# Performance work log

Hardware: AMD Instinct MI355X
Metric: run time of the kernel (lower is better)

Reference implementation:

```python
import jax, jax.numpy as jnp
import numpy as np

N_NODES = 100000
N_EDGES = 2000000
IN_C = 64
OUT_C = 64
K = 27
G = 4


def setup_inputs() -> dict:
    key = jax.random.key(0)
    k1, k2, k3, k4, k5, k6 = jax.random.split(key, 6)
    inp = {
        "input": jax.random.normal(k1, (N_NODES, IN_C), dtype=jnp.float32),
        "i": jax.random.randint(k2, (N_EDGES,), 0, N_NODES),
        "j": jax.random.randint(k3, (N_EDGES,), 0, N_NODES),
        "k": jax.random.randint(k4, (N_EDGES,), 0, K),
        "n": N_NODES,
        "weight": jax.random.normal(k5, (IN_C, OUT_C // G, K), dtype=jnp.float32) * 0.1,
        "bias": jax.random.normal(k6, (OUT_C,), dtype=jnp.float32) * 0.1,
    }
    return inp


def reference(input, i, j, k, n, weight, bias):
    # weight: [in_c, out_c//g, K] -> w: [K, g, in_c//g, out_c//g]
    w = weight.reshape(G, IN_C // G, OUT_C // G, K).transpose(3, 0, 1, 2)
    x3 = input.reshape(input.shape[0], G, IN_C // G)  # [n, g, c]
    # Transform every node by every kernel-position weight once (n*K small GEMMs)
    # instead of materializing a per-edge [E,g,c,d] weight gather.
    x_all = jnp.einsum('ngc,kgcd->nkgd', x3, w)  # [n, K, g, d]
    msgs = x_all[j, k]                            # [E, g, d] gather per edge
    out = jax.ops.segment_sum(msgs, i, num_segments=n)  # scatter-add to dst nodes
    out = out.reshape(-1, OUT_C) + bias
    return out
```

## Files before the change

### kernel.cpp

```cpp
#include <hip/hip_runtime.h>
#include <hip/hip_bf16.h>


#define KPOS 27
#define WPACK_UINTS (KPOS * 512)
#define SCAN_NB 256

typedef unsigned u32x4 __attribute__((ext_vector_type(4)));

__device__ __forceinline__ unsigned packbf(float a, float b) {
    unsigned ua = (unsigned)__bfloat16_as_ushort(__float2bfloat16(a));
    unsigned ub = (unsigned)__bfloat16_as_ushort(__float2bfloat16(b));
    return ua | (ub << 16);
}

#define DOT2(A, X, W) asm("v_dot2_f32_bf16 %0, %1, %2, %0" : "+v"(A) : "v"(X), "v"(W))

__global__ void init_out_kernel(float* __restrict__ out, const float* __restrict__ bias, int total) {
    int idx = blockIdx.x * blockDim.x + threadIdx.x;
    if (idx < total) out[idx] = bias[idx & 63];
}
__global__ void edge_kernel_rawW(const float* __restrict__ input, const int* __restrict__ ei,
                                 const int* __restrict__ ej, const int* __restrict__ ek,
                                 const float* __restrict__ weight, float* __restrict__ out, int n_edges) {
    const int lane = threadIdx.x & 63;
    const int g16 = lane & 48;
    const int d = lane & 15;
    int wave = (blockIdx.x * blockDim.x + threadIdx.x) >> 6;
    int n_waves = (gridDim.x * blockDim.x) >> 6;
    for (int e = wave; e < n_edges; e += n_waves) {
        int ie = ei[e], je = ej[e], ke = ek[e];
        float x = input[je * 64 + lane];
        float acc = 0.0f;
        #pragma unroll
        for (int c = 0; c < 16; ++c)
            acc += __shfl(x, g16 + c, 64) * weight[(g16 + c) * 432 + d * 27 + ke];
        atomicAdd(out + ie * 64 + lane, acc);
    }
}

__global__ void prep_kernel(const float* __restrict__ input, const float* __restrict__ weight,
                            unsigned* __restrict__ xb, unsigned* __restrict__ wp,
                            int* __restrict__ cnt, int n_nodes, int nquads) {
    int t = blockIdx.x * blockDim.x + threadIdx.x;
    if (t < n_nodes) cnt[t] = 0;
    if (t < WPACK_UINTS) {
        int k  = t >> 9;
        int r  = t & 511;
        int q  = r >> 8;
        int r2 = r & 255;
        int gc = r2 >> 2;
        int m  = r2 & 3;
        int g = gc >> 4, d = gc & 15;
        int c = (q * 4 + m) * 2;
        int ic = g * 16 + c;
        float f0 = weight[ic * 432 + d * 27 + k];
        float f1 = weight[(ic + 1) * 432 + d * 27 + k];
        wp[t] = packbf(f0, f1);
    }
    if (t < nquads) {
        const float4* in4 = (const float4*)input;
        float4 a = in4[2 * t], b = in4[2 * t + 1];
        uint4 o;
        o.x = packbf(a.x, a.y);
        o.y = packbf(a.z, a.w);
        o.z = packbf(b.x, b.y);
        o.w = packbf(b.z, b.w);
        ((uint4*)xb)[t] = o;
    }
}

__global__ void rank_kernel(const int* __restrict__ ei, int* __restrict__ cnt,
                            unsigned short* __restrict__ rank, int n_edges) {
    int e = blockIdx.x * blockDim.x + threadIdx.x;
    if (e < n_edges)
        rank[e] = (unsigned short)atomicAdd(&cnt[ei[e]], 1);
}

__global__ void scanA_kernel(const int* __restrict__ cnt, int* __restrict__ partial,
                             int n, int chunk) {
    __shared__ int red[256];
    int b = blockIdx.x;
    int lo = b * chunk, hi = min(lo + chunk, n);
    int s = 0;
    for (int v = lo + threadIdx.x; v < hi; v += 256) s += cnt[v];
    red[threadIdx.x] = s;
    __syncthreads();
    for (int d = 128; d > 0; d >>= 1) {
        if (threadIdx.x < d) red[threadIdx.x] += red[threadIdx.x + d];
        __syncthreads();
    }
    if (threadIdx.x == 0) partial[b] = red[0];
}

__global__ void scanB_kernel(int* __restrict__ partial, int* __restrict__ off, int n) {
    __shared__ int sums[SCAN_NB];
    int t = threadIdx.x;
    sums[t] = partial[t];
    __syncthreads();
    for (int d = 1; d < SCAN_NB; d <<= 1) {
        int val = (t >= d) ? sums[t - d] : 0;
        __syncthreads();
        sums[t] += val;
        __syncthreads();
    }
    partial[t] = (t == 0) ? 0 : sums[t - 1];
    if (t == SCAN_NB - 1) off[n] = sums[t];
}

__global__ void scanC_kernel(const int* __restrict__ cnt, const int* __restrict__ partial,
                             int* __restrict__ off, int n, int chunk) {
    __shared__ int excl[256];
    int b = blockIdx.x;
    int lo = b * chunk, hi = min(lo + chunk, n);
    int per = (chunk + 255) >> 8;
    int tlo = lo + threadIdx.x * per;
    int thi = min(tlo + per, hi);
    int s = 0;
    for (int v = tlo; v < thi; ++v) s += cnt[v];
    excl[threadIdx.x] = s;
    __syncthreads();
    for (int d = 1; d < 256; d <<= 1) {
        int val = (threadIdx.x >= d) ? excl[threadIdx.x - d] : 0;
        __syncthreads();
        excl[threadIdx.x] += val;
        __syncthreads();
    }
    int run = partial[b] + ((threadIdx.x == 0) ? 0 : excl[threadIdx.x - 1]);
    for (int v = tlo; v < thi; ++v) { off[v] = run; run += cnt[v]; }
}

__global__ void fill_kernel(const int* __restrict__ ei, const int* __restrict__ ej,
                            const int* __restrict__ ek, const int* __restrict__ off,
                            const unsigned short* __restrict__ rank,
                            unsigned* __restrict__ jk, int n_edges) {
    int e = blockIdx.x * blockDim.x + threadIdx.x;
    if (e < n_edges)
        jk[off[ei[e]] + (int)rank[e]] = (unsigned)ej[e] | ((unsigned)ek[e] << 17);
}

__launch_bounds__(1024, 8)
__global__ void gather_kernel(const unsigned* __restrict__ xb,
                              const unsigned* __restrict__ jk,
                              const int* __restrict__ off,
                              const unsigned* __restrict__ wp,
                              const float* __restrict__ bias,
                              float* __restrict__ out, int n) {
    __shared__ unsigned lds[WPACK_UINTS];
    for (int t = threadIdx.x; t < WPACK_UINTS / 4; t += blockDim.x)
        ((uint4*)lds)[t] = ((const uint4*)wp)[t];
    __syncthreads();

    const int lane = threadIdx.x & 63;
    const int g8   = (lane & 48) >> 1;
    const float b  = bias[lane];
    const unsigned* wl = lds + (lane << 2);

    int wid = (blockIdx.x * blockDim.x + threadIdx.x) >> 6;
    int nw  = (gridDim.x * blockDim.x) >> 6;

#define XISSUE(P0, P1, XA, XC, XB2, XD) do {                                     \
        const u32x4* xp0_ = (const u32x4*)(xb + (((P0) & 0x1FFFFu) << 5) + g8);  \
        const u32x4* xp1_ = (const u32x4*)(xb + (((P1) & 0x1FFFFu) << 5) + g8);  \
        XA  = xp0_[0]; XC = xp0_[1];                                             \
        XB2 = xp1_[0]; XD = xp1_[1];                                             \
    } while (0)

#define PAIR_EDGE(XA, XC, PV, AL, AH) do {                                       \
        const u32x4* wr_ = (const u32x4*)(wl + (((PV) >> 17) << 9));             \
        u32x4 wa_ = wr_[0], wb_ = wr_[64];                                       \
        DOT2(AL, XA[0], wa_[0]); DOT2(AH, XA[1], wa_[1]);                        \
        DOT2(AL, XA[2], wa_[2]); DOT2(AH, XA[3], wa_[3]);                        \
        DOT2(AL, XC[0], wb_[0]); DOT2(AH, XC[1], wb_[1]);                        \
        DOT2(AL, XC[2], wb_[2]); DOT2(AH, XC[3], wb_[3]);                        \
    } while (0)

    for (int v = wid; v < n; v += nw) {
        int e0 = off[v];
        int e1 = off[v + 1];
        int nE = e1 - e0;
        int P  = nE >> 1;
        float a0l = 0.0f, a0h = 0.0f, a1l = 0.0f, a1h = 0.0f;

        if (P > 0) {
            unsigned pc0 = jk[e0], pc1 = jk[e0 + 1];
            u32x4 Aa, Ac, Ab, Ad;
            XISSUE(pc0, pc1, Aa, Ac, Ab, Ad);
            unsigned pn0 = pc0, pn1 = pc1;
            if (P > 1) { pn0 = jk[e0 + 2]; pn1 = jk[e0 + 3]; }
            u32x4 Ba, Bc, Bb, Bd;

            int t = 0;
            for (; t + 2 <= P; t += 2) {
                unsigned pf0 = pn0, pf1 = pn1;
                if (t + 2 < P) { pf0 = jk[e0 + 2 * t + 4]; pf1 = jk[e0 + 2 * t + 5]; }
                XISSUE(pn0, pn1, Ba, Bc, Bb, Bd);
                PAIR_EDGE(Aa, Ac, pc0, a0l, a0h);
                PAIR_EDGE(Ab, Ad, pc1, a1l, a1h);
                pc0 = pn0; pc1 = pn1; pn0 = pf0; pn1 = pf1;
                unsigned pg0 = pn0, pg1 = pn1;
                if (t + 3 < P) { pg0 = jk[e0 + 2 * t + 6]; pg1 = jk[e0 + 2 * t + 7]; }
                if (t + 2 < P) XISSUE(pn0, pn1, Aa, Ac, Ab, Ad);
                PAIR_EDGE(Ba, Bc, pc0, a0l, a0h);
                PAIR_EDGE(Bb, Bd, pc1, a1l, a1h);
                pc0 = pn0; pc1 = pn1; pn0 = pg0; pn1 = pg1;
            }
            if (t < P) {
                PAIR_EDGE(Aa, Ac, pc0, a0l, a0h);
                PAIR_EDGE(Ab, Ad, pc1, a1l, a1h);
            }
        }

        if (nE & 1) {
            unsigned p_ = jk[e1 - 1];
            const u32x4* xr_ = (const u32x4*)(xb + ((p_ & 0x1FFFFu) << 5) + g8);
            u32x4 xa_ = xr_[0], xc_ = xr_[1];
            PAIR_EDGE(xa_, xc_, p_, a0l, a0h);
        }

        out[(v << 6) + lane] = (a0l + a0h) + (a1l + a1h) + b;
    }
#undef XISSUE
#undef PAIR_EDGE
}

static inline size_t al256(size_t x) { return (x + 255) & ~(size_t)255; }

extern "C" void kernel_launch(void* const* d_in, const int* in_sizes, int n_in,
                              void* d_out, int out_size, void* d_ws, size_t ws_size,
                              hipStream_t stream) {
    const float* input  = (const float*)d_in[0];
    const int*   ei     = (const int*)d_in[1];
    const int*   ej     = (const int*)d_in[2];
    const int*   ek     = (const int*)d_in[3];
    const float* weight = (const float*)d_in[5];
    const float* bias   = (const float*)d_in[6];

    const int n_edges = in_sizes[1];
    const int n_nodes = out_size / 64;

    size_t off_o  = 0;
    size_t off_s  = al256((size_t)(n_nodes + 1) * 4);
    size_t cnt_o  = off_o + off_s;
    size_t cnt_s  = al256((size_t)n_nodes * 4);
    size_t par_o  = cnt_o + cnt_s;
    size_t par_s  = al256((size_t)SCAN_NB * 4);
    size_t rank_o = par_o + par_s;
    size_t rank_s = al256((size_t)n_edges * 2);
    size_t jk_o   = rank_o + rank_s;
    size_t jk_s   = al256((size_t)n_edges * 4);
    size_t wp_o   = jk_o + jk_s;
    size_t wp_s   = al256((size_t)WPACK_UINTS * 4);
    size_t xb_o   = wp_o + wp_s;
    size_t xb_s   = al256((size_t)n_nodes * 64 * 2);
    size_t need   = xb_o + xb_s;

    if (ws_size < need) {
        int blocks = (out_size + 255) / 256;
        hipLaunchKernelGGL(init_out_kernel, dim3(blocks), dim3(256), 0, stream,
                           (float*)d_out, bias, out_size);
        hipLaunchKernelGGL(edge_kernel_rawW, dim3(2048), dim3(256), 0, stream,
                           input, ei, ej, ek, weight, (float*)d_out, n_edges);
        return;
    }

    char* ws = (char*)d_ws;
    int*            off  = (int*)(ws + off_o);
    int*            cnt  = (int*)(ws + cnt_o);
    int*            par  = (int*)(ws + par_o);
    unsigned short* rank = (unsigned short*)(ws + rank_o);
    unsigned*       jk   = (unsigned*)(ws + jk_o);
    unsigned*       wp   = (unsigned*)(ws + wp_o);
    unsigned*       xb   = (unsigned*)(ws + xb_o);

    const int eb = (n_edges + 255) / 256;
    const int nquads = n_nodes * 8;
    const int prep_range = max(nquads, max(n_nodes, WPACK_UINTS));
    const int chunk = (n_nodes + SCAN_NB - 1) / SCAN_NB;

    hipLaunchKernelGGL(prep_kernel, dim3((prep_range + 255) / 256), dim3(256), 0, stream,
                       input, weight, xb, wp, cnt, n_nodes, nquads);
    hipLaunchKernelGGL(rank_kernel, dim3(eb), dim3(256), 0, stream, ei, cnt, rank, n_edges);
    hipLaunchKernelGGL(scanA_kernel, dim3(SCAN_NB), dim3(256), 0, stream, cnt, par, n_nodes, chunk);
    hipLaunchKernelGGL(scanB_kernel, dim3(1), dim3(SCAN_NB), 0, stream, par, off, n_nodes);
    hipLaunchKernelGGL(scanC_kernel, dim3(SCAN_NB), dim3(256), 0, stream, cnt, par, off, n_nodes, chunk);
    hipLaunchKernelGGL(fill_kernel, dim3(eb), dim3(256), 0, stream, ei, ej, ek, off, rank, jk, n_edges);

    hipLaunchKernelGGL(gather_kernel, dim3(512), dim3(1024), 0, stream,
                       xb, jk, off, wp, bias, (float*)d_out, n_nodes);
}
```

Baseline: 304.5 us.

## Bucket edges by destination block and kernel position, accumulate in LDS

Edges are now counting-sorted into buckets keyed by (destination node block of 128, kernel position) instead of by destination node. Each 512-thread gather block owns 128 destination nodes and keeps a 128x64 fp32 accumulator in LDS. Its waves walk the block's edges grouped by kernel position, so each weight slice is loaded into registers once per run rather than reread from LDS per edge. Partial sums go to LDS through shared-memory atomics, then bias is added and the tile is written out with coalesced stores. The trade is LDS atomic contention in place of register accumulation, plus per-edge load imbalance across blocks.

New measurement: 978.7 us. 3.21x slower.

```diff
diff --git a/kernel.cpp b/kernel.cpp
--- a/kernel.cpp
+++ b/kernel.cpp
@@ -3,6 +3,7 @@
 
 
 #define KPOS 27
+#define NB 128
 #define WPACK_UINTS (KPOS * 512)
 #define SCAN_NB 256
 
@@ -41,9 +42,9 @@
 
 __global__ void prep_kernel(const float* __restrict__ input, const float* __restrict__ weight,
                             unsigned* __restrict__ xb, unsigned* __restrict__ wp,
-                            int* __restrict__ cnt, int n_nodes, int nquads) {
+                            int* __restrict__ cnt, int nbk, int nquads) {
     int t = blockIdx.x * blockDim.x + threadIdx.x;
-    if (t < n_nodes) cnt[t] = 0;
+    if (t < nbk) cnt[t] = 0;
     if (t < WPACK_UINTS) {
         int k  = t >> 9;
         int r  = t & 511;
@@ -70,11 +71,14 @@
     }
 }
 
-__global__ void rank_kernel(const int* __restrict__ ei, int* __restrict__ cnt,
+__global__ void rank_kernel(const int* __restrict__ ei, const int* __restrict__ ek,
+                            int* __restrict__ cnt,
                             unsigned short* __restrict__ rank, int n_edges) {
     int e = blockIdx.x * blockDim.x + threadIdx.x;
-    if (e < n_edges)
-        rank[e] = (unsigned short)atomicAdd(&cnt[ei[e]], 1);
+    if (e < n_edges) {
+        int bkt = (ei[e] >> 7) * KPOS + ek[e];
+        rank[e] = (unsigned short)atomicAdd(&cnt[bkt], 1);
+    }
 }
 
 __global__ void scanA_kernel(const int* __restrict__ cnt, int* __restrict__ partial,
@@ -133,95 +137,111 @@
 __global__ void fill_kernel(const int* __restrict__ ei, const int* __restrict__ ej,
                             const int* __restrict__ ek, const int* __restrict__ off,
                             const unsigned short* __restrict__ rank,
-                            unsigned* __restrict__ jk, int n_edges) {
+                            unsigned* __restrict__ recs, int n_edges) {
     int e = blockIdx.x * blockDim.x + threadIdx.x;
-    if (e < n_edges)
-        jk[off[ei[e]] + (int)rank[e]] = (unsigned)ej[e] | ((unsigned)ek[e] << 17);
-}
-
-__launch_bounds__(1024, 8)
+    if (e < n_edges) {
+        int ie = ei[e];
+        int bkt = (ie >> 7) * KPOS + ek[e];
+        recs[off[bkt] + (int)rank[e]] = (unsigned)ej[e] | (((unsigned)ie & (NB - 1)) << 17);
+    }
+}
+
+__launch_bounds__(512, 8)
 __global__ void gather_kernel(const unsigned* __restrict__ xb,
-                              const unsigned* __restrict__ jk,
-                              const int* __restrict__ off,
+                              const unsigned* __restrict__ recs,
+                              const int* __restrict__ boff,
                               const unsigned* __restrict__ wp,
                               const float* __restrict__ bias,
-                              float* __restrict__ out, int n) {
-    __shared__ unsigned lds[WPACK_UINTS];
-    for (int t = threadIdx.x; t < WPACK_UINTS / 4; t += blockDim.x)
-        ((uint4*)lds)[t] = ((const uint4*)wp)[t];
-    __syncthreads();
+                              float* __restrict__ out, int n_nodes) {
+    __shared__ float acc[NB * 64];
+    for (int t = threadIdx.x; t < NB * 16; t += blockDim.x)
+        ((float4*)acc)[t] = make_float4(0.f, 0.f, 0.f, 0.f);
+    __syncthreads();
+
+    const int b = blockIdx.x;
+    const int* bo = boff + b * KPOS;
+    const int seg1 = bo[KPOS];
 
     const int lane = threadIdx.x & 63;
-    const int g8   = (lane & 48) >> 1;
-    const float b  = bias[lane];
-    const unsigned* wl = lds + (lane << 2);
-
-    int wid = (blockIdx.x * blockDim.x + threadIdx.x) >> 6;
-    int nw  = (gridDim.x * blockDim.x) >> 6;
-
-#define XISSUE(P0, P1, XA, XC, XB2, XD) do {                                     \
-        const u32x4* xp0_ = (const u32x4*)(xb + (((P0) & 0x1FFFFu) << 5) + g8);  \
-        const u32x4* xp1_ = (const u32x4*)(xb + (((P1) & 0x1FFFFu) << 5) + g8);  \
-        XA  = xp0_[0]; XC = xp0_[1];                                             \
-        XB2 = xp1_[0]; XD = xp1_[1];                                             \
-    } while (0)
-
-#define PAIR_EDGE(XA, XC, PV, AL, AH) do {                                       \
-        const u32x4* wr_ = (const u32x4*)(wl + (((PV) >> 17) << 9));             \
-        u32x4 wa_ = wr_[0], wb_ = wr_[64];                                       \
-        DOT2(AL, XA[0], wa_[0]); DOT2(AH, XA[1], wa_[1]);                        \
-        DOT2(AL, XA[2], wa_[2]); DOT2(AH, XA[3], wa_[3]);                        \
-        DOT2(AL, XC[0], wb_[0]); DOT2(AH, XC[1], wb_[1]);                        \
-        DOT2(AL, XC[2], wb_[2]); DOT2(AH, XC[3], wb_[3]);                        \
-    } while (0)
-
-    for (int v = wid; v < n; v += nw) {
-        int e0 = off[v];
-        int e1 = off[v + 1];
-        int nE = e1 - e0;
-        int P  = nE >> 1;
-        float a0l = 0.0f, a0h = 0.0f, a1l = 0.0f, a1h = 0.0f;
-
-        if (P > 0) {
-            unsigned pc0 = jk[e0], pc1 = jk[e0 + 1];
-            u32x4 Aa, Ac, Ab, Ad;
-            XISSUE(pc0, pc1, Aa, Ac, Ab, Ad);
-            unsigned pn0 = pc0, pn1 = pc1;
-            if (P > 1) { pn0 = jk[e0 + 2]; pn1 = jk[e0 + 3]; }
-            u32x4 Ba, Bc, Bb, Bd;
-
-            int t = 0;
-            for (; t + 2 <= P; t += 2) {
-                unsigned pf0 = pn0, pf1 = pn1;
-                if (t + 2 < P) { pf0 = jk[e0 + 2 * t + 4]; pf1 = jk[e0 + 2 * t + 5]; }
-                XISSUE(pn0, pn1, Ba, Bc, Bb, Bd);
-                PAIR_EDGE(Aa, Ac, pc0, a0l, a0h);
-                PAIR_EDGE(Ab, Ad, pc1, a1l, a1h);
-                pc0 = pn0; pc1 = pn1; pn0 = pf0; pn1 = pf1;
-                unsigned pg0 = pn0, pg1 = pn1;
-                if (t + 3 < P) { pg0 = jk[e0 + 2 * t + 6]; pg1 = jk[e0 + 2 * t + 7]; }
-                if (t + 2 < P) XISSUE(pn0, pn1, Aa, Ac, Ab, Ad);
-                PAIR_EDGE(Ba, Bc, pc0, a0l, a0h);
-                PAIR_EDGE(Bb, Bd, pc1, a1l, a1h);
-                pc0 = pn0; pc1 = pn1; pn0 = pg0; pn1 = pg1;
-            }
-            if (t < P) {
-                PAIR_EDGE(Aa, Ac, pc0, a0l, a0h);
-                PAIR_EDGE(Ab, Ad, pc1, a1l, a1h);
+    const int half = lane >> 5;
+    const int g    = (lane >> 3) & 3;
+    const int dp   = lane & 7;
+    const int g8u  = g << 3;
+    const int och  = (g << 4) + dp;
+    const unsigned wbase = (unsigned)(och << 2);
+
+    const int wv  = threadIdx.x >> 6;
+    const int nwv = blockDim.x >> 6;
+    const int seg0 = bo[0];
+    const int len  = seg1 - seg0;
+    const int per  = (len + nwv - 1) / nwv;
+    const int p0   = seg0 + wv * per;
+    const int p1   = min(p0 + per, seg1);
+
+    if (p0 < p1) {
+        int k = 0;
+        while (k < KPOS - 1 && bo[k + 1] <= p0) ++k;
+        for (; k < KPOS; ++k) {
+            int r0 = max(p0, bo[k]);
+            int r1 = min(p1, bo[k + 1]);
+            if (r0 >= p1) break;
+            if (r0 >= r1) continue;
+            const u32x4* wq = (const u32x4*)(wp + (k << 9) + wbase);
+            u32x4 w00 = wq[0], w01 = wq[64], w10 = wq[8], w11 = wq[72];
+            for (int p = r0; p < r1; p += 4) {
+                int i0 = p + half, i1 = p + 2 + half;
+                bool v0 = i0 < r1, v1 = i1 < r1;
+                unsigned rec0 = recs[v0 ? i0 : r1 - 1];
+                unsigned rec1 = recs[v1 ? i1 : r1 - 1];
+                const u32x4* xp0 = (const u32x4*)(xb + ((rec0 & 0x1FFFFu) << 5) + g8u);
+                const u32x4* xp1 = (const u32x4*)(xb + ((rec1 & 0x1FFFFu) << 5) + g8u);
+                u32x4 xa0 = xp0[0], xc0 = xp0[1];
+                u32x4 xa1 = xp1[0], xc1 = xp1[1];
+
+                float s0 = 0.f, s1 = 0.f;
+                DOT2(s0, xa0[0], w00[0]); DOT2(s0, xa0[1], w00[1]);
+                DOT2(s0, xa0[2], w00[2]); DOT2(s0, xa0[3], w00[3]);
+                DOT2(s0, xc0[0], w01[0]); DOT2(s0, xc0[1], w01[1]);
+                DOT2(s0, xc0[2], w01[2]); DOT2(s0, xc0[3], w01[3]);
+                DOT2(s1, xa0[0], w10[0]); DOT2(s1, xa0[1], w10[1]);
+                DOT2(s1, xa0[2], w10[2]); DOT2(s1, xa0[3], w10[3]);
+                DOT2(s1, xc0[0], w11[0]); DOT2(s1, xc0[1], w11[1]);
+                DOT2(s1, xc0[2], w11[2]); DOT2(s1, xc0[3], w11[3]);
+                if (v0) {
+                    int il = (int)(rec0 >> 17);
+                    atomicAdd(&acc[(il << 6) + och], s0);
+                    atomicAdd(&acc[(il << 6) + och + 8], s1);
+                }
+
+                float t0 = 0.f, t1 = 0.f;
+                DOT2(t0, xa1[0], w00[0]); DOT2(t0, xa1[1], w00[1]);
+                DOT2(t0, xa1[2], w00[2]); DOT2(t0, xa1[3], w00[3]);
+                DOT2(t0, xc1[0], w01[0]); DOT2(t0, xc1[1], w01[1]);
+                DOT2(t0, xc1[2], w01[2]); DOT2(t0, xc1[3], w01[3]);
+                DOT2(t1, xa1[0], w10[0]); DOT2(t1, xa1[1], w10[1]);
+                DOT2(t1, xa1[2], w10[2]); DOT2(t1, xa1[3], w10[3]);
+                DOT2(t1, xc1[0], w11[0]); DOT2(t1, xc1[1], w11[1]);
+                DOT2(t1, xc1[2], w11[2]); DOT2(t1, xc1[3], w11[3]);
+                if (v1) {
+                    int il = (int)(rec1 >> 17);
+                    atomicAdd(&acc[(il << 6) + och], t0);
+                    atomicAdd(&acc[(il << 6) + och + 8], t1);
+                }
             }
         }
-
-        if (nE & 1) {
-            unsigned p_ = jk[e1 - 1];
-            const u32x4* xr_ = (const u32x4*)(xb + ((p_ & 0x1FFFFu) << 5) + g8);
-            u32x4 xa_ = xr_[0], xc_ = xr_[1];
-            PAIR_EDGE(xa_, xc_, p_, a0l, a0h);
+    }
+    __syncthreads();
+
+    const int base = b * NB;
+    for (int t = threadIdx.x; t < NB * 16; t += blockDim.x) {
+        int node = base + (t >> 4);
+        if (node < n_nodes) {
+            float4 v = ((float4*)acc)[t];
+            float4 bb = ((const float4*)bias)[t & 15];
+            v.x += bb.x; v.y += bb.y; v.z += bb.z; v.w += bb.w;
+            ((float4*)out)[(node << 4) + (t & 15)] = v;
         }
-
-        out[(v << 6) + lane] = (a0l + a0h) + (a1l + a1h) + b;
-    }
-#undef XISSUE
-#undef PAIR_EDGE
+    }
 }
 
 static inline size_t al256(size_t x) { return (x + 255) & ~(size_t)255; }
@@ -238,18 +258,20 @@
 
     const int n_edges = in_sizes[1];
     const int n_nodes = out_size / 64;
+    const int nblocks = (n_nodes + NB - 1) / NB;
+    const int nbk     = nblocks * KPOS;
 
     size_t off_o  = 0;
-    size_t off_s  = al256((size_t)(n_nodes + 1) * 4);
+    size_t off_s  = al256((size_t)(nbk + 1) * 4);
     size_t cnt_o  = off_o + off_s;
-    size_t cnt_s  = al256((size_t)n_nodes * 4);
+    size_t cnt_s  = al256((size_t)nbk * 4);
     size_t par_o  = cnt_o + cnt_s;
     size_t par_s  = al256((size_t)SCAN_NB * 4);
     size_t rank_o = par_o + par_s;
     size_t rank_s = al256((size_t)n_edges * 2);
-    size_t jk_o   = rank_o + rank_s;
-    size_t jk_s   = al256((size_t)n_edges * 4);
-    size_t wp_o   = jk_o + jk_s;
+    size_t rec_o  = rank_o + rank_s;
+    size_t rec_s  = al256((size_t)n_edges * 4);
+    size_t wp_o   = rec_o + rec_s;
     size_t wp_s   = al256((size_t)WPACK_UINTS * 4);
     size_t xb_o   = wp_o + wp_s;
     size_t xb_s   = al256((size_t)n_nodes * 64 * 2);
@@ -269,23 +291,23 @@
     int*            cnt  = (int*)(ws + cnt_o);
     int*            par  = (int*)(ws + par_o);
     unsigned short* rank = (unsigned short*)(ws + rank_o);
-    unsigned*       jk   = (unsigned*)(ws + jk_o);
+    unsigned*       recs = (unsigned*)(ws + rec_o);
     unsigned*       wp   = (unsigned*)(ws + wp_o);
     unsigned*       xb   = (unsigned*)(ws + xb_o);
 
     const int eb = (n_edges + 255) / 256;
     const int nquads = n_nodes * 8;
-    const int prep_range = max(nquads, max(n_nodes, WPACK_UINTS));
-    const int chunk = (n_nodes + SCAN_NB - 1) / SCAN_NB;
+    const int prep_range = max(nquads, max(nbk, WPACK_UINTS));
+    const int chunk = (nbk + SCAN_NB - 1) / SCAN_NB;
 
     hipLaunchKernelGGL(prep_kernel, dim3((prep_range + 255) / 256), dim3(256), 0, stream,
-                       input, weight, xb, wp, cnt, n_nodes, nquads);
-    hipLaunchKernelGGL(rank_kernel, dim3(eb), dim3(256), 0, stream, ei, cnt, rank, n_edges);
-    hipLaunchKernelGGL(scanA_kernel, dim3(SCAN_NB), dim3(256), 0, stream, cnt, par, n_nodes, chunk);
-    hipLaunchKernelGGL(scanB_kernel, dim3(1), dim3(SCAN_NB), 0, stream, par, off, n_nodes);
-    hipLaunchKernelGGL(scanC_kernel, dim3(SCAN_NB), dim3(256), 0, stream, cnt, par, off, n_nodes, chunk);
-    hipLaunchKernelGGL(fill_kernel, dim3(eb), dim3(256), 0, stream, ei, ej, ek, off, rank, jk, n_edges);
-
-    hipLaunchKernelGGL(gather_kernel, dim3(512), dim3(1024), 0, stream,
-                       xb, jk, off, wp, bias, (float*)d_out, n_nodes);
-}
+                       input, weight, xb, wp, cnt, nbk, nquads);
+    hipLaunchKernelGGL(rank_kernel, dim3(eb), dim3(256), 0, stream, ei, ek, cnt, rank, n_edges);
+    hipLaunchKernelGGL(scanA_kernel, dim3(SCAN_NB), dim3(256), 0, stream, cnt, par, nbk, chunk);
+    hipLaunchKernelGGL(scanB_kernel, dim3(1), dim3(SCAN_NB), 0, stream, par, off, nbk);
+    hipLaunchKernelGGL(scanC_kernel, dim3(SCAN_NB), dim3(256), 0, stream, cnt, par, off, nbk, chunk);
+    hipLaunchKernelGGL(fill_kernel, dim3(eb), dim3(256), 0, stream, ei, ej, ek, off, rank, recs, n_edges);
+
+    hipLaunchKernelGGL(gather_kernel, dim3(nblocks), dim3(512), 0, stream,
+                       xb, recs, off, wp, bias, (float*)d_out, n_nodes);
+}
```
